# Kernel tuning notes

Hardware: AMD Instinct MI355X
Metric: run time of the kernel (lower is better)

## Reference

```python
import jax, jax.numpy as jnp
import numpy as np

THR = 10.0           # spike threshold (all layers, igarss2023 config)
LEAK1, LEAK2, LEAK3 = 9.0, 1.0, 0.0  # subtractive leak per layer
POOL1_K, POOL1_S = 7, 6
POOL2_K, POOL2_S = 2, 2
WTA_BLOCK = 2        # local spatial WTA window


def conv2d_same(x, w):
    # x: (B,C,H,W), w: (O,I,kh,kw)
    return jax.lax.conv_general_dilated(
        x, w, window_strides=(1, 1), padding='SAME',
        dimension_numbers=('NCHW', 'OIHW', 'NCHW'))


def maxpool(x, k, s):
    return jax.lax.reduce_window(
        x, -jnp.inf, jax.lax.max, (1, 1, k, k), (1, 1, s, s), 'VALID')


def wta(mem, spk, block=WTA_BLOCK):
    """Winner-take-all lateral inhibition ('both' mode):
    (1) channel competition: only the channel with max membrane at each
        spatial location may spike; (2) local spatial competition: only the
        max-membrane neuron within each block x block window of each map
        may spike. Requires H,W divisible by block."""
    C = mem.shape[1]
    ch_win = jnp.argmax(mem, axis=1)                         # (B,H,W)
    ch_mask = jax.nn.one_hot(ch_win, C, axis=1, dtype=mem.dtype)  # (B,C,H,W)
    loc = jax.lax.reduce_window(
        mem, -jnp.inf, jax.lax.max,
        (1, 1, block, block), (1, 1, block, block), 'VALID')
    loc_up = jnp.repeat(jnp.repeat(loc, block, axis=2), block, axis=3)
    sp_mask = (mem >= loc_up).astype(mem.dtype)
    return spk * ch_mask * sp_mask


def lif_step(mem, inp, leak, use_wta):
    # integrate -> threshold -> WTA -> reset-to-zero -> subtractive leak
    mem = mem + inp
    spk = (mem >= THR).astype(mem.dtype)
    if use_wta:
        spk = wta(mem, spk)
    mem = jnp.where(spk > 0, 0.0, mem)
    mem = jnp.maximum(mem - leak, 0.0)
    return mem, spk


def setup_inputs() -> dict:
    key = jax.random.key(0)
    k0, k1, k2, k3 = jax.random.split(key, 4)
    T, B, H, W = 20, 8, 256, 256
    x = jax.random.uniform(k0, (T, B, 1, H, W), dtype=jnp.float32)
    # STDP-style weights are non-negative in [0,1)
    w1 = jax.random.uniform(k1, (4, 1, 5, 5), dtype=jnp.float32)
    w2 = jax.random.uniform(k2, (36, 4, 5, 5), dtype=jnp.float32)
    w3 = jax.random.uniform(k3, (1, 36, 7, 7), dtype=jnp.float32)
    return {"x": x, "w1": w1, "w2": w2, "w3": w3}


def reference(x, w1, w2, w3):
    T, B, _, H, W = x.shape
    H1, W1 = H, W                                   # conv1 SAME
    H2 = (H1 - POOL1_K) // POOL1_S + 1              # 42
    W2 = (W1 - POOL1_K) // POOL1_S + 1
    H3 = (H2 - POOL2_K) // POOL2_S + 1              # 21
    W3 = (W2 - POOL2_K) // POOL2_S + 1
    C1, C2, C3 = w1.shape[0], w2.shape[0], w3.shape[0]

    m1_0 = jnp.zeros((B, C1, H1, W1), x.dtype)
    m2_0 = jnp.zeros((B, C2, H2, W2), x.dtype)
    m3_0 = jnp.zeros((B, C3, H3, W3), x.dtype)

    def step(carry, xt):
        m1, m2, m3 = carry
        m1, s1 = lif_step(m1, conv2d_same(xt, w1), LEAK1, True)
        p1 = maxpool(s1, POOL1_K, POOL1_S)
        m2, s2 = lif_step(m2, conv2d_same(p1, w2), LEAK2, True)
        p2 = maxpool(s2, POOL2_K, POOL2_S)
        m3, s3 = lif_step(m3, conv2d_same(p2, w3), LEAK3, False)
        return (m1, m2, m3), s3

    _, cls_spikes = jax.lax.scan(step, (m1_0, m2_0, m3_0), x)
    return cls_spikes  # (T, B, n_classes, H3, W3)
```

## Files before the change

### kernel.cpp

```cpp
#include <hip/hip_runtime.h>
#include <stdint.h>

#define THR 10.0f
#define AGT __HIP_MEMORY_SCOPE_AGENT

static constexpr size_t OFF_P2  = 2097152;
static constexpr size_t OFF_BAR = 2359296;

static __device__ __forceinline__ uint64_t ldu64(const uint64_t* p) {
    return __hip_atomic_load(p, __ATOMIC_RELAXED, AGT);
}
static __device__ __forceinline__ void stu64(uint64_t* p, uint64_t v) {
    __hip_atomic_store(p, v, __ATOMIC_RELAXED, AGT);
}

__global__ __launch_bounds__(256) void zero_bar(uint32_t* __restrict__ bar) {
    if (threadIdx.x < 256) bar[threadIdx.x] = 0u;
}

__device__ __forceinline__ void gbar(uint32_t* bar, int bid, uint32_t n) {
    __syncthreads();
    if (threadIdx.x == 0) {
        uint32_t* base = bar + (bid >> 6) * 32;
        uint32_t a = __hip_atomic_fetch_add(base, 1u, __ATOMIC_RELAXED, AGT);
        if (a == 64u * n - 1u)
            __hip_atomic_fetch_add(base + 16, 1u, __ATOMIC_RELAXED, AGT);
        while (__hip_atomic_load(base + 16, __ATOMIC_RELAXED, AGT) < n)
            __builtin_amdgcn_s_sleep(2);
    }
    __syncthreads();
}

__global__ __launch_bounds__(256, 2) void spike_persist(
    const float* __restrict__ x,
    const float* __restrict__ w1,
    const float* __restrict__ w2,
    const float* __restrict__ w3,
    float* __restrict__ out,
    uint8_t* __restrict__ s1b,
    uint8_t* __restrict__ p2b,
    uint32_t* __restrict__ bar)
{
    __shared__ union {
        float    xs[2112];
        uint64_t st64[279];
    } u;
    __shared__ uint64_t p2s[441];
    __shared__ float    ps[400];
    __shared__ float    mem_s[1296];
    __shared__ float    bm_s[324];
    __shared__ int      wc_s[36];
    __shared__ uint32_t p2a[18];

    const int tid = threadIdx.x;
    const int bid = blockIdx.x;
    uint32_t nbar = 0;

    const int b1 = bid >> 6;
    const int r0 = (bid & 63) * 4;
    const int tr = tid >> 7, tc = tid & 127;

    const int tIdx = bid & 63;
    const int b2 = bid >> 6;
    const int tyi = tIdx >> 3, txi = tIdx & 7;
    const int oy2 = tyi < 5 ? 6 * tyi : 30 + 4 * (tyi - 5);
    const int ox2 = txi < 5 ? 6 * txi : 30 + 4 * (txi - 5);
    const int th2 = tyi < 5 ? 6 : 4;
    const int tw2 = txi < 5 ? 6 : 4;
    const int wave = tid >> 6, lane = tid & 63;
    const int pr = lane / 6, pc = lane - 6 * pr;
    const bool act = (pr < th2) && (pc < tw2);
    const int prA = pr > 5 ? 0 : pr, pcA = pc;

    const int lid3 = (bid & 63) * 4 + wave;
    const int kyl = lane / 7, kxl = lane % 7;

    float w3v[36];
#pragma unroll
    for (int c = 0; c < 36; c++) w3v[c] = (lane < 49) ? w3[c * 49 + lane] : 0.f;

    int aoff[9]; uint32_t avalm = 0;
#pragma unroll
    for (int i = 0; i < 9; i++) {
        int idx = tid + i * 256;
        int row = idx / 264, col = idx - row * 264;
        int gy = r0 + row - 2, gx = col - 2;
        if ((idx < 2112) && gy >= 0 && gy < 256 && gx >= 0 && gx < 256)
            avalm |= 1u << i;
        aoff[i] = gy * 256 + gx;
    }
    const int s1soff64 = (b1 * 128 + (r0 >> 1) + tr) * 32 + (tc >> 2);

    const int rb0 = 3 * oy2 - 6;
    const int cb0 = (3 * ox2 - 6) >> 1;
    const int cq0 = cb0 >> 1;
    const int d16 = 2 * (cb0 & 1);
    int boff[2]; uint32_t bvalm = 0;
#pragma unroll
    for (int i = 0; i < 2; i++) {
        int idx = tid + i * 256;
        int row = idx / 9, q = idx - 9 * row;
        int grow = rb0 + row;
        int ucol = 2 * (cq0 + q);
        if ((idx < 279) && grow >= 0 && grow < 128 && ucol >= 0 && ucol < 64)
            bvalm |= 1u << i;
        boff[i] = (b2 * 128 + grow) * 32 + cq0 + q;
    }

    bool l3in[2], l3v[2]; int l3o[2];
#pragma unroll
    for (int rep = 0; rep < 2; rep++) {
        int o = lid3 + rep * 256;
        int rr = o / 21, cl = o - rr * 21;
        int yy = rr + kyl - 3, xx = cl + kxl - 3;
        l3in[rep] = o < 441;
        l3v[rep] = (o < 441) && (lane < 49) && yy >= 0 && yy < 21 && xx >= 0 && xx < 21;
        l3o[rep] = yy * 21 + xx;
    }

    float m1r[4][2][2];
#pragma unroll
    for (int c = 0; c < 4; c++)
#pragma unroll
        for (int dy = 0; dy < 2; dy++)
#pragma unroll
            for (int dx = 0; dx < 2; dx++) m1r[c][dy][dx] = 0.f;
    float m2r[9];
#pragma unroll
    for (int i = 0; i < 9; i++) m2r[i] = 0.f;
    float m3r[2] = {0.f, 0.f};

    for (int k = 0; k < 7; k++) {
        for (int tt = 0; tt < 4; tt++) {
            const int t = 4 * k + tt;
            if (t < 20) {
                uint64_t* s1w = reinterpret_cast<uint64_t*>(s1b + (size_t)(t & 7) * 262144);
                const float* xb = x + ((size_t)t * 8 + b1) * 65536;
                __syncthreads();
#pragma unroll
                for (int i = 0; i < 9; i++) {
                    int idx = tid + i * 256;
                    if (idx < 2112) u.xs[idx] = ((avalm >> i) & 1u) ? xb[aoff[i]] : 0.f;
                }
                __syncthreads();

                const float2* xs2 = reinterpret_cast<const float2*>(u.xs);
                float p[6][6];
#pragma unroll
                for (int i = 0; i < 6; i++)
#pragma unroll
                    for (int j = 0; j < 3; j++) {
                        float2 v = xs2[(2 * tr + i) * 132 + tc + j];
                        p[i][2 * j] = v.x; p[i][2 * j + 1] = v.y;
                    }

                float acc[4][2][2];
#pragma unroll
                for (int c = 0; c < 4; c++)
#pragma unroll
                    for (int dy = 0; dy < 2; dy++)
#pragma unroll
                        for (int dx = 0; dx < 2; dx++) acc[c][dy][dx] = 0.f;
#pragma unroll
                for (int c = 0; c < 4; c++)
#pragma unroll
                    for (int ky = 0; ky < 5; ky++)
#pragma unroll
                        for (int kx = 0; kx < 5; kx++) {
                            float w = w1[c * 25 + ky * 5 + kx];
#pragma unroll
                            for (int dy = 0; dy < 2; dy++)
#pragma unroll
                                for (int dx = 0; dx < 2; dx++)
                                    acc[c][dy][dx] = fmaf(p[dy + ky][dx + kx], w, acc[c][dy][dx]);
                        }

                float mem[4][2][2];
#pragma unroll
                for (int c = 0; c < 4; c++)
#pragma unroll
                    for (int dy = 0; dy < 2; dy++)
#pragma unroll
                        for (int dx = 0; dx < 2; dx++)
                            mem[c][dy][dx] = m1r[c][dy][dx] + acc[c][dy][dx];

                int wc[2][2];
#pragma unroll
                for (int dy = 0; dy < 2; dy++)
#pragma unroll
                    for (int dx = 0; dx < 2; dx++) {
                        int w = 0; float mx = mem[0][dy][dx];
#pragma unroll
                        for (int c = 1; c < 4; c++) {
                            float v = mem[c][dy][dx];
                            if (v > mx) { mx = v; w = c; }
                        }
                        wc[dy][dx] = w;
                    }

                float bm[4];
#pragma unroll
                for (int c = 0; c < 4; c++)
                    bm[c] = fmaxf(fmaxf(mem[c][0][0], mem[c][0][1]),
                                  fmaxf(mem[c][1][0], mem[c][1][1]));

                uint32_t bits = 0;
#pragma unroll
                for (int c = 0; c < 4; c++)
#pragma unroll
                    for (int dy = 0; dy < 2; dy++)
#pragma unroll
                        for (int dx = 0; dx < 2; dx++) {
                            float m = mem[c][dy][dx];
                            bool s = (m >= THR) && (wc[dy][dx] == c) && (m >= bm[c]);
                            m1r[c][dy][dx] = fmaxf((s ? 0.f : m) - 9.0f, 0.f);
                            bits |= (s ? 1u : 0u) << (c * 4 + dy * 2 + dx);
                        }
                uint32_t b32 = bits | ((uint32_t)__shfl_xor((int)bits, 1, 64) << 16);
                uint64_t b64 = (uint64_t)b32 |
                               ((uint64_t)(uint32_t)__shfl_xor((int)b32, 2, 64) << 32);
                if (!(tid & 3)) stu64(s1w + s1soff64, b64);
            }
        }

        uint64_t pf0 = 0, pf1 = 0;
        {
            int tb0 = 4 * k - 4;
            if (tb0 >= 0 && tb0 < 20) {
                const uint64_t* s1r64 = reinterpret_cast<const uint64_t*>(
                    s1b + (size_t)(tb0 & 7) * 262144);
                pf0 = (bvalm & 1u) ? ldu64(s1r64 + boff[0]) : 0ull;
                pf1 = (bvalm & 2u) ? ldu64(s1r64 + boff[1]) : 0ull;
            }
        }

        for (int tt = 0; tt < 4; tt++) {
            const int tl = 4 * k - 8 + tt;
            if (tl >= 0 && tl < 20) {
                const uint64_t* pb64 = reinterpret_cast<const uint64_t*>(
                    p2b + (size_t)(tl & 7) * 32768) + b2 * 441;
                __syncthreads();
                if (tid < 441) p2s[tid] = ldu64(pb64 + tid);
                {
                    int idx2 = tid + 256;
                    if (idx2 < 441) p2s[idx2] = ldu64(pb64 + idx2);
                }
                __syncthreads();
#pragma unroll
                for (int rep = 0; rep < 2; rep++) {
                    if (l3in[rep]) {
                        int o = lid3 + rep * 256;
                        uint64_t v = l3v[rep] ? p2s[l3o[rep]] : 0ull;
                        uint32_t lo = (uint32_t)v, hi = (uint32_t)(v >> 32);
                        float accv = 0.f;
#pragma unroll
                        for (int c = 0; c < 32; c++) accv += ((lo >> c) & 1u) ? w3v[c] : 0.f;
#pragma unroll
                        for (int c = 0; c < 4; c++)  accv += ((hi >> c) & 1u) ? w3v[32 + c] : 0.f;
#pragma unroll
                        for (int off = 32; off; off >>= 1) accv += __shfl_xor(accv, off, 64);
                        float memv3 = m3r[rep] + accv;
                        bool s = memv3 >= THR;
                        if (lane == 0) out[(size_t)tl * 3528 + b2 * 441 + o] = s ? 1.f : 0.f;
                        m3r[rep] = fmaxf(s ? 0.f : memv3, 0.f);
                    }
                }
            }
        }

        for (int tt = 0; tt < 4; tt++) {
            const int tb = 4 * k - 4 + tt;
            if (tb >= 0 && tb < 20) {
                uint64_t* p2w64 = reinterpret_cast<uint64_t*>(p2b + (size_t)(tb & 7) * 32768);

                __syncthreads();
                u.st64[tid] = pf0;
                {
                    int idx2 = tid + 256;
                    if (idx2 < 279) u.st64[idx2] = pf1;
                }
                {
                    int tbn = tb + 1;
                    if (tt < 3 && tbn < 20) {
                        const uint64_t* s1r64 = reinterpret_cast<const uint64_t*>(
                            s1b + (size_t)(tbn & 7) * 262144);
                        pf0 = (bvalm & 1u) ? ldu64(s1r64 + boff[0]) : 0ull;
                        pf1 = (bvalm & 2u) ? ldu64(s1r64 + boff[1]) : 0ull;
                    }
                }
                if (tid < 18) p2a[tid] = 0;
                __syncthreads();

                if (tid < 100) {
                    int r = tid / 10, cc2 = tid - 10 * (tid / 10);
                    int gy = oy2 - 2 + r, gx = ox2 - 2 + cc2;
                    uint32_t accb = 0;
                    if (r < th2 + 4 && cc2 < tw2 + 4 && gy >= 0 && gy < 42 && gx >= 0 && gx < 42) {
                        const uint16_t* st16 = reinterpret_cast<const uint16_t*>(u.st64);
#pragma unroll
                        for (int kr = 0; kr < 4; kr++)
#pragma unroll
                            for (int kc = 0; kc < 4; kc++) {
                                uint32_t m = (kr < 3) ? (kc < 3 ? 0xFu : 0x5u)
                                                      : (kc < 3 ? 0x3u : 0x1u);
                                uint32_t v = st16[(3 * r + kr) * 36 + 3 * cc2 + kc + d16];
                                accb |= v & (m * 0x1111u);
                            }
                    }
#pragma unroll
                    for (int ic = 0; ic < 4; ic++)
                        ps[ic * 100 + tid] = ((accb >> (4 * ic)) & 0xFu) ? 1.f : 0.f;
                }
                __syncthreads();

                float pv[4][5][5];
#pragma unroll
                for (int ic = 0; ic < 4; ic++)
#pragma unroll
                    for (int i = 0; i < 5; i++)
#pragma unroll
                        for (int j = 0; j < 5; j++)
                            pv[ic][i][j] = ps[ic * 100 + (prA + i) * 10 + (pcA + j)];

                float memv[9];
                for (int cc = 0; cc < 9; cc++) {
                    int c = cc * 4 + wave;
                    const float* wr = w2 + (size_t)__builtin_amdgcn_readfirstlane(c) * 100;
                    float accv = 0.f;
#pragma unroll
                    for (int ic = 0; ic < 4; ic++)
#pragma unroll
                        for (int i = 0; i < 5; i++)
#pragma unroll
                            for (int j = 0; j < 5; j++)
                                accv = fmaf(pv[ic][i][j], wr[ic * 25 + i * 5 + j], accv);
                    float m = act ? (m2r[cc] + accv) : -1e30f;
                    memv[cc] = m;
                    if (lane < 36) mem_s[c * 36 + lane] = m;
                }
                __syncthreads();

                if (tid < 36) {
                    float mx = mem_s[tid]; int w = 0;
#pragma unroll
                    for (int c = 1; c < 36; c++) {
                        float v = mem_s[c * 36 + tid];
                        if (v > mx) { mx = v; w = c; }
                    }
                    wc_s[tid] = w;
                }
#pragma unroll
                for (int i = 0; i < 2; i++) {
                    int idx = tid + i * 256;
                    if (idx < 324) {
                        int c = idx / 9, blk = idx - 9 * c;
                        int br = blk / 3, bc2 = blk - 3 * br;
                        int l0 = 12 * br + 2 * bc2;
                        float a = mem_s[c * 36 + l0],     bb2 = mem_s[c * 36 + l0 + 1];
                        float d = mem_s[c * 36 + l0 + 6], e   = mem_s[c * 36 + l0 + 7];
                        bm_s[idx] = fmaxf(fmaxf(a, bb2), fmaxf(d, e));
                    }
                }
                __syncthreads();

                const int blkl = (pr >> 1) * 3 + (pc >> 1);
                for (int cc = 0; cc < 9; cc++) {
                    int c = cc * 4 + wave;
                    if (act) {
                        float m = memv[cc];
                        bool s = (m >= THR) && (wc_s[lane] == c) && (m >= bm_s[c * 9 + blkl]);
                        m2r[cc] = fmaxf((s ? 0.f : m) - 1.0f, 0.f);
                    }
                }

#pragma unroll
                for (int i = 0; i < 2; i++) {
                    int idx = tid + i * 256;
                    if (idx < 324) {
                        int c = idx / 9, blk = idx - 9 * c;
                        int br = blk / 3, bc2 = blk - 3 * br;
                        if (2 * br < th2 && 2 * bc2 < tw2) {
                            int l0 = 12 * br + 2 * bc2;
                            float bmv = bm_s[idx];
                            bool any = false;
#pragma unroll
                            for (int kk = 0; kk < 4; kk++) {
                                int l = l0 + (kk >> 1) * 6 + (kk & 1);
                                float m = mem_s[c * 36 + l];
                                any |= (m >= THR) && (wc_s[l] == c) && (m >= bmv);
                            }
                            if (any)
                                atomicOr(&p2a[(blk << 1) + (c >> 5)], 1u << (c & 31));
                        }
                    }
                }
                __syncthreads();

                if (tid < 9) {
                    int br = tid / 3, bc2 = tid - 3 * br;
                    if (2 * br < th2 && 2 * bc2 < tw2) {
                        int cell = b2 * 441 + ((oy2 >> 1) + br) * 21 + (ox2 >> 1) + bc2;
                        uint64_t v = (uint64_t)p2a[tid * 2] |
                                     ((uint64_t)p2a[tid * 2 + 1] << 32);
                        stu64(p2w64 + cell, v);
                    }
                }
            }
        }

        if (k < 6) gbar(bar, bid, ++nbar);
    }
}

extern "C" void kernel_launch(void* const* d_in, const int* in_sizes, int n_in,
                              void* d_out, int out_size, void* d_ws, size_t ws_size,
                              hipStream_t stream) {
    const float* x  = (const float*)d_in[0];
    const float* w1 = (const float*)d_in[1];
    const float* w2 = (const float*)d_in[2];
    const float* w3 = (const float*)d_in[3];
    float* out = (float*)d_out;
    uint8_t* s1 = (uint8_t*)d_ws;
    uint8_t* p2 = (uint8_t*)d_ws + OFF_P2;
    uint32_t* bar = (uint32_t*)((char*)d_ws + OFF_BAR);

    zero_bar<<<1, 256, 0, stream>>>(bar);

    void* args[] = {(void*)&x, (void*)&w1, (void*)&w2, (void*)&w3,
                    (void*)&out, (void*)&s1, (void*)&p2, (void*)&bar};
    hipLaunchCooperativeKernel((void*)spike_persist, dim3(512), dim3(256),
                               args, 0, stream);
}
```

Before: 410.3 us.

## Warp-specialize persistent kernel so layer-1 and layer-2 stages run concurrently

Block size doubles to 512 threads. The first 256 threads handle layer-1 convolution and LIF plus layer-3 readout, and the second 256 handle layer-2 pooling, convolution and WTA. Each timestep interleaves both halves under shared __syncthreads, so stages that used to run one after another in the same block now overlap. Layer 3 now reads p2 straight from global memory instead of staging it in LDS, and the shared-memory union is split into separate buffers. This raises register and LDS pressure, and it adds barriers that both halves must hit even when only one half has work.

```diff
diff --git a/kernel.cpp b/kernel.cpp
--- a/kernel.cpp
+++ b/kernel.cpp
@@ -31,7 +31,7 @@
     __syncthreads();
 }
 
-__global__ __launch_bounds__(256, 2) void spike_persist(
+__global__ __launch_bounds__(512, 4) void spike_persist(
     const float* __restrict__ x,
     const float* __restrict__ w1,
     const float* __restrict__ w2,
@@ -41,11 +41,8 @@
     uint8_t* __restrict__ p2b,
     uint32_t* __restrict__ bar)
 {
-    __shared__ union {
-        float    xs[2112];
-        uint64_t st64[279];
-    } u;
-    __shared__ uint64_t p2s[441];
+    __shared__ float    xs[2112];
+    __shared__ uint64_t st64[279];
     __shared__ float    ps[400];
     __shared__ float    mem_s[1296];
     __shared__ float    bm_s[324];
@@ -54,97 +51,119 @@
 
     const int tid = threadIdx.x;
     const int bid = blockIdx.x;
+    const int bt = bid >> 6;
+    const bool isA = tid < 256;
+    const int btid = tid & 255;
+    const int wv = (tid >> 6) & 3;
+    const int lane = tid & 63;
     uint32_t nbar = 0;
 
-    const int b1 = bid >> 6;
-    const int r0 = (bid & 63) * 4;
-    const int tr = tid >> 7, tc = tid & 127;
-
-    const int tIdx = bid & 63;
-    const int b2 = bid >> 6;
-    const int tyi = tIdx >> 3, txi = tIdx & 7;
-    const int oy2 = tyi < 5 ? 6 * tyi : 30 + 4 * (tyi - 5);
-    const int ox2 = txi < 5 ? 6 * txi : 30 + 4 * (txi - 5);
-    const int th2 = tyi < 5 ? 6 : 4;
-    const int tw2 = txi < 5 ? 6 : 4;
-    const int wave = tid >> 6, lane = tid & 63;
-    const int pr = lane / 6, pc = lane - 6 * pr;
-    const bool act = (pr < th2) && (pc < tw2);
-    const int prA = pr > 5 ? 0 : pr, pcA = pc;
-
-    const int lid3 = (bid & 63) * 4 + wave;
-    const int kyl = lane / 7, kxl = lane % 7;
-
-    float w3v[36];
-#pragma unroll
-    for (int c = 0; c < 36; c++) w3v[c] = (lane < 49) ? w3[c * 49 + lane] : 0.f;
-
-    int aoff[9]; uint32_t avalm = 0;
-#pragma unroll
-    for (int i = 0; i < 9; i++) {
-        int idx = tid + i * 256;
-        int row = idx / 264, col = idx - row * 264;
-        int gy = r0 + row - 2, gx = col - 2;
-        if ((idx < 2112) && gy >= 0 && gy < 256 && gx >= 0 && gx < 256)
-            avalm |= 1u << i;
-        aoff[i] = gy * 256 + gx;
+    float m1r[4][2][2];
+    int aoff[9]; uint32_t avalm = 0; int s1soff64 = 0;
+    float w3v[36]; float m3r[2] = {0.f, 0.f};
+    bool l3in[2], l3v[2]; int l3o[2]; int lid3 = 0;
+    float m2r[9];
+    int boff[2]; uint32_t bvalm = 0; int d16 = 0;
+    int oy2 = 0, ox2 = 0, th2 = 0, tw2 = 0;
+    bool act = false; int prA = 0, pcA = 0;
+    uint64_t pf0 = 0, pf1 = 0;
+
+    if (isA) {
+        const int r0 = (bid & 63) * 4;
+        const int tr = tid >> 7, tc = tid & 127;
+#pragma unroll
+        for (int c = 0; c < 4; c++)
+#pragma unroll
+            for (int dy = 0; dy < 2; dy++)
+#pragma unroll
+                for (int dx = 0; dx < 2; dx++) m1r[c][dy][dx] = 0.f;
+#pragma unroll
+        for (int i = 0; i < 9; i++) {
+            int idx = tid + i * 256;
+            int row = idx / 264, col = idx - row * 264;
+            int gy = r0 + row - 2, gx = col - 2;
+            if ((idx < 2112) && gy >= 0 && gy < 256 && gx >= 0 && gx < 256)
+                avalm |= 1u << i;
+            aoff[i] = gy * 256 + gx;
+        }
+        s1soff64 = (bt * 128 + (r0 >> 1) + tr) * 32 + (tc >> 2);
+#pragma unroll
+        for (int c = 0; c < 36; c++) w3v[c] = (lane < 49) ? w3[c * 49 + lane] : 0.f;
+        lid3 = (bid & 63) * 4 + wv;
+        const int kyl = lane / 7, kxl = lane % 7;
+#pragma unroll
+        for (int rep = 0; rep < 2; rep++) {
+            int o = lid3 + rep * 256;
+            int rr = o / 21, cl = o - rr * 21;
+            int yy = rr + kyl - 3, xx = cl + kxl - 3;
+            l3in[rep] = o < 441;
+            l3v[rep] = (o < 441) && (lane < 49) && yy >= 0 && yy < 21 && xx >= 0 && xx < 21;
+            l3o[rep] = bt * 441 + yy * 21 + xx;
+        }
+    } else {
+        const int tIdx = bid & 63;
+        const int tyi = tIdx >> 3, txi = tIdx & 7;
+        oy2 = tyi < 5 ? 6 * tyi : 30 + 4 * (tyi - 5);
+        ox2 = txi < 5 ? 6 * txi : 30 + 4 * (txi - 5);
+        th2 = tyi < 5 ? 6 : 4;
+        tw2 = txi < 5 ? 6 : 4;
+        const int pr = lane / 6, pc = lane - 6 * pr;
+        act = (pr < th2) && (pc < tw2);
+        prA = pr > 5 ? 0 : pr; pcA = pc;
+#pragma unroll
+        for (int i = 0; i < 9; i++) m2r[i] = 0.f;
+        const int rb0 = 3 * oy2 - 6;
+        const int cb0 = (3 * ox2 - 6) >> 1;
+        const int cq0 = cb0 >> 1;
+        d16 = 2 * (cb0 & 1);
+#pragma unroll
+        for (int i = 0; i < 2; i++) {
+            int idx = btid + i * 256;
+            int row = idx / 9, q = idx - 9 * row;
+            int grow = rb0 + row;
+            int ucol = 2 * (cq0 + q);
+            if ((idx < 279) && grow >= 0 && grow < 128 && ucol >= 0 && ucol < 64)
+                bvalm |= 1u << i;
+            boff[i] = (bt * 128 + grow) * 32 + cq0 + q;
+        }
     }
-    const int s1soff64 = (b1 * 128 + (r0 >> 1) + tr) * 32 + (tc >> 2);
-
-    const int rb0 = 3 * oy2 - 6;
-    const int cb0 = (3 * ox2 - 6) >> 1;
-    const int cq0 = cb0 >> 1;
-    const int d16 = 2 * (cb0 & 1);
-    int boff[2]; uint32_t bvalm = 0;
-#pragma unroll
-    for (int i = 0; i < 2; i++) {
-        int idx = tid + i * 256;
-        int row = idx / 9, q = idx - 9 * row;
-        int grow = rb0 + row;
-        int ucol = 2 * (cq0 + q);
-        if ((idx < 279) && grow >= 0 && grow < 128 && ucol >= 0 && ucol < 64)
-            bvalm |= 1u << i;
-        boff[i] = (b2 * 128 + grow) * 32 + cq0 + q;
-    }
-
-    bool l3in[2], l3v[2]; int l3o[2];
-#pragma unroll
-    for (int rep = 0; rep < 2; rep++) {
-        int o = lid3 + rep * 256;
-        int rr = o / 21, cl = o - rr * 21;
-        int yy = rr + kyl - 3, xx = cl + kxl - 3;
-        l3in[rep] = o < 441;
-        l3v[rep] = (o < 441) && (lane < 49) && yy >= 0 && yy < 21 && xx >= 0 && xx < 21;
-        l3o[rep] = yy * 21 + xx;
-    }
-
-    float m1r[4][2][2];
-#pragma unroll
-    for (int c = 0; c < 4; c++)
-#pragma unroll
-        for (int dy = 0; dy < 2; dy++)
-#pragma unroll
-            for (int dx = 0; dx < 2; dx++) m1r[c][dy][dx] = 0.f;
-    float m2r[9];
-#pragma unroll
-    for (int i = 0; i < 9; i++) m2r[i] = 0.f;
-    float m3r[2] = {0.f, 0.f};
 
     for (int k = 0; k < 7; k++) {
+        if (!isA) {
+            int tb0 = 4 * k - 4;
+            if (tb0 >= 0 && tb0 < 20) {
+                const uint64_t* s1r64 = reinterpret_cast<const uint64_t*>(
+                    s1b + (size_t)(tb0 & 7) * 262144);
+                pf0 = (bvalm & 1u) ? ldu64(s1r64 + boff[0]) : 0ull;
+                pf1 = (bvalm & 2u) ? ldu64(s1r64 + boff[1]) : 0ull;
+            }
+        }
+
         for (int tt = 0; tt < 4; tt++) {
             const int t = 4 * k + tt;
-            if (t < 20) {
-                uint64_t* s1w = reinterpret_cast<uint64_t*>(s1b + (size_t)(t & 7) * 262144);
-                const float* xb = x + ((size_t)t * 8 + b1) * 65536;
-                __syncthreads();
+            const int tb = 4 * k - 4 + tt;
+            const int tl = 4 * k - 8 + tt;
+            const bool tok = t < 20;
+            const bool tbok = (tb >= 0) && (tb < 20);
+            const bool tlok = (tl >= 0) && (tl < 20);
+
+            if (isA && tok) {
+                const float* xb = x + ((size_t)t * 8 + bt) * 65536;
 #pragma unroll
                 for (int i = 0; i < 9; i++) {
                     int idx = tid + i * 256;
-                    if (idx < 2112) u.xs[idx] = ((avalm >> i) & 1u) ? xb[aoff[i]] : 0.f;
-                }
-                __syncthreads();
-
-                const float2* xs2 = reinterpret_cast<const float2*>(u.xs);
+                    if (idx < 2112) xs[idx] = ((avalm >> i) & 1u) ? xb[aoff[i]] : 0.f;
+                }
+            } else if (!isA && tbok) {
+                st64[btid] = pf0;
+                if (btid + 256 < 279) st64[btid + 256] = pf1;
+            }
+            __syncthreads();
+
+            if (isA && tok) {
+                uint64_t* s1w = reinterpret_cast<uint64_t*>(s1b + (size_t)(t & 7) * 262144);
+                const int tr = tid >> 7, tc = tid & 127;
+                const float2* xs2 = reinterpret_cast<const float2*>(xs);
                 float p[6][6];
 #pragma unroll
                 for (int i = 0; i < 6; i++)
@@ -220,83 +239,13 @@
                 uint64_t b64 = (uint64_t)b32 |
                                ((uint64_t)(uint32_t)__shfl_xor((int)b32, 2, 64) << 32);
                 if (!(tid & 3)) stu64(s1w + s1soff64, b64);
-            }
-        }
-
-        uint64_t pf0 = 0, pf1 = 0;
-        {
-            int tb0 = 4 * k - 4;
-            if (tb0 >= 0 && tb0 < 20) {
-                const uint64_t* s1r64 = reinterpret_cast<const uint64_t*>(
-                    s1b + (size_t)(tb0 & 7) * 262144);
-                pf0 = (bvalm & 1u) ? ldu64(s1r64 + boff[0]) : 0ull;
-                pf1 = (bvalm & 2u) ? ldu64(s1r64 + boff[1]) : 0ull;
-            }
-        }
-
-        for (int tt = 0; tt < 4; tt++) {
-            const int tl = 4 * k - 8 + tt;
-            if (tl >= 0 && tl < 20) {
-                const uint64_t* pb64 = reinterpret_cast<const uint64_t*>(
-                    p2b + (size_t)(tl & 7) * 32768) + b2 * 441;
-                __syncthreads();
-                if (tid < 441) p2s[tid] = ldu64(pb64 + tid);
-                {
-                    int idx2 = tid + 256;
-                    if (idx2 < 441) p2s[idx2] = ldu64(pb64 + idx2);
-                }
-                __syncthreads();
-#pragma unroll
-                for (int rep = 0; rep < 2; rep++) {
-                    if (l3in[rep]) {
-                        int o = lid3 + rep * 256;
-                        uint64_t v = l3v[rep] ? p2s[l3o[rep]] : 0ull;
-                        uint32_t lo = (uint32_t)v, hi = (uint32_t)(v >> 32);
-                        float accv = 0.f;
-#pragma unroll
-                        for (int c = 0; c < 32; c++) accv += ((lo >> c) & 1u) ? w3v[c] : 0.f;
-#pragma unroll
-                        for (int c = 0; c < 4; c++)  accv += ((hi >> c) & 1u) ? w3v[32 + c] : 0.f;
-#pragma unroll
-                        for (int off = 32; off; off >>= 1) accv += __shfl_xor(accv, off, 64);
-                        float memv3 = m3r[rep] + accv;
-                        bool s = memv3 >= THR;
-                        if (lane == 0) out[(size_t)tl * 3528 + b2 * 441 + o] = s ? 1.f : 0.f;
-                        m3r[rep] = fmaxf(s ? 0.f : memv3, 0.f);
-                    }
-                }
-            }
-        }
-
-        for (int tt = 0; tt < 4; tt++) {
-            const int tb = 4 * k - 4 + tt;
-            if (tb >= 0 && tb < 20) {
-                uint64_t* p2w64 = reinterpret_cast<uint64_t*>(p2b + (size_t)(tb & 7) * 32768);
-
-                __syncthreads();
-                u.st64[tid] = pf0;
-                {
-                    int idx2 = tid + 256;
-                    if (idx2 < 279) u.st64[idx2] = pf1;
-                }
-                {
-                    int tbn = tb + 1;
-                    if (tt < 3 && tbn < 20) {
-                        const uint64_t* s1r64 = reinterpret_cast<const uint64_t*>(
-                            s1b + (size_t)(tbn & 7) * 262144);
-                        pf0 = (bvalm & 1u) ? ldu64(s1r64 + boff[0]) : 0ull;
-                        pf1 = (bvalm & 2u) ? ldu64(s1r64 + boff[1]) : 0ull;
-                    }
-                }
-                if (tid < 18) p2a[tid] = 0;
-                __syncthreads();
-
-                if (tid < 100) {
-                    int r = tid / 10, cc2 = tid - 10 * (tid / 10);
+            } else if (!isA && tbok) {
+                if (btid < 100) {
+                    int r = btid / 10, cc2 = btid - 10 * (btid / 10);
                     int gy = oy2 - 2 + r, gx = ox2 - 2 + cc2;
                     uint32_t accb = 0;
                     if (r < th2 + 4 && cc2 < tw2 + 4 && gy >= 0 && gy < 42 && gx >= 0 && gx < 42) {
-                        const uint16_t* st16 = reinterpret_cast<const uint16_t*>(u.st64);
+                        const uint16_t* st16 = reinterpret_cast<const uint16_t*>(st64);
 #pragma unroll
                         for (int kr = 0; kr < 4; kr++)
 #pragma unroll
@@ -309,10 +258,34 @@
                     }
 #pragma unroll
                     for (int ic = 0; ic < 4; ic++)
-                        ps[ic * 100 + tid] = ((accb >> (4 * ic)) & 0xFu) ? 1.f : 0.f;
-                }
-                __syncthreads();
-
+                        ps[ic * 100 + btid] = ((accb >> (4 * ic)) & 0xFu) ? 1.f : 0.f;
+                }
+            }
+            __syncthreads();
+
+            if (isA && tlok) {
+                const uint64_t* pb64 = reinterpret_cast<const uint64_t*>(
+                    p2b + (size_t)(tl & 7) * 32768);
+#pragma unroll
+                for (int rep = 0; rep < 2; rep++) {
+                    if (l3in[rep]) {
+                        int o = lid3 + rep * 256;
+                        uint64_t v = l3v[rep] ? ldu64(pb64 + l3o[rep]) : 0ull;
+                        uint32_t lo = (uint32_t)v, hi = (uint32_t)(v >> 32);
+                        float accv = 0.f;
+#pragma unroll
+                        for (int c = 0; c < 32; c++) accv += ((lo >> c) & 1u) ? w3v[c] : 0.f;
+#pragma unroll
+                        for (int c = 0; c < 4; c++)  accv += ((hi >> c) & 1u) ? w3v[32 + c] : 0.f;
+#pragma unroll
+                        for (int off = 32; off; off >>= 1) accv += __shfl_xor(accv, off, 64);
+                        float memv3 = m3r[rep] + accv;
+                        bool s = memv3 >= THR;
+                        if (lane == 0) out[(size_t)tl * 3528 + bt * 441 + o] = s ? 1.f : 0.f;
+                        m3r[rep] = fmaxf(s ? 0.f : memv3, 0.f);
+                    }
+                }
+            } else if (!isA && tbok) {
                 float pv[4][5][5];
 #pragma unroll
                 for (int ic = 0; ic < 4; ic++)
@@ -322,9 +295,18 @@
                         for (int j = 0; j < 5; j++)
                             pv[ic][i][j] = ps[ic * 100 + (prA + i) * 10 + (pcA + j)];
 
-                float memv[9];
+                {
+                    int tbn = tb + 1;
+                    if (tt < 3 && tbn >= 0 && tbn < 20) {
+                        const uint64_t* s1r64 = reinterpret_cast<const uint64_t*>(
+                            s1b + (size_t)(tbn & 7) * 262144);
+                        pf0 = (bvalm & 1u) ? ldu64(s1r64 + boff[0]) : 0ull;
+                        pf1 = (bvalm & 2u) ? ldu64(s1r64 + boff[1]) : 0ull;
+                    }
+                }
+
                 for (int cc = 0; cc < 9; cc++) {
-                    int c = cc * 4 + wave;
+                    int c = cc * 4 + wv;
                     const float* wr = w2 + (size_t)__builtin_amdgcn_readfirstlane(c) * 100;
                     float accv = 0.f;
 #pragma unroll
@@ -335,23 +317,24 @@
                             for (int j = 0; j < 5; j++)
                                 accv = fmaf(pv[ic][i][j], wr[ic * 25 + i * 5 + j], accv);
                     float m = act ? (m2r[cc] + accv) : -1e30f;
-                    memv[cc] = m;
                     if (lane < 36) mem_s[c * 36 + lane] = m;
                 }
-                __syncthreads();
-
-                if (tid < 36) {
-                    float mx = mem_s[tid]; int w = 0;
+            }
+            __syncthreads();
+
+            if (!isA && tbok) {
+                if (btid < 36) {
+                    float mx = mem_s[btid]; int w = 0;
 #pragma unroll
                     for (int c = 1; c < 36; c++) {
-                        float v = mem_s[c * 36 + tid];
+                        float v = mem_s[c * 36 + btid];
                         if (v > mx) { mx = v; w = c; }
                     }
-                    wc_s[tid] = w;
+                    wc_s[btid] = w;
                 }
 #pragma unroll
                 for (int i = 0; i < 2; i++) {
-                    int idx = tid + i * 256;
+                    int idx = btid + i * 256;
                     if (idx < 324) {
                         int c = idx / 9, blk = idx - 9 * c;
                         int br = blk / 3, bc2 = blk - 3 * br;
@@ -361,21 +344,24 @@
                         bm_s[idx] = fmaxf(fmaxf(a, bb2), fmaxf(d, e));
                     }
                 }
-                __syncthreads();
-
+                if (btid < 18) p2a[btid] = 0;
+            }
+            __syncthreads();
+
+            if (!isA && tbok) {
+                const int pr = lane / 6, pc = lane - 6 * pr;
                 const int blkl = (pr >> 1) * 3 + (pc >> 1);
                 for (int cc = 0; cc < 9; cc++) {
-                    int c = cc * 4 + wave;
+                    int c = cc * 4 + wv;
                     if (act) {
-                        float m = memv[cc];
+                        float m = mem_s[c * 36 + lane];
                         bool s = (m >= THR) && (wc_s[lane] == c) && (m >= bm_s[c * 9 + blkl]);
                         m2r[cc] = fmaxf((s ? 0.f : m) - 1.0f, 0.f);
                     }
                 }
-
 #pragma unroll
                 for (int i = 0; i < 2; i++) {
-                    int idx = tid + i * 256;
+                    int idx = btid + i * 256;
                     if (idx < 324) {
                         int c = idx / 9, blk = idx - 9 * c;
                         int br = blk / 3, bc2 = blk - 3 * br;
@@ -394,14 +380,18 @@
                         }
                     }
                 }
-                __syncthreads();
-
-                if (tid < 9) {
-                    int br = tid / 3, bc2 = tid - 3 * br;
+            }
+            __syncthreads();
+
+            if (!isA && tbok) {
+                if (btid < 9) {
+                    int br = btid / 3, bc2 = btid - 3 * br;
                     if (2 * br < th2 && 2 * bc2 < tw2) {
-                        int cell = b2 * 441 + ((oy2 >> 1) + br) * 21 + (ox2 >> 1) + bc2;
-                        uint64_t v = (uint64_t)p2a[tid * 2] |
-                                     ((uint64_t)p2a[tid * 2 + 1] << 32);
+                        uint64_t* p2w64 = reinterpret_cast<uint64_t*>(
+                            p2b + (size_t)(tb & 7) * 32768);
+                        int cell = bt * 441 + ((oy2 >> 1) + br) * 21 + (ox2 >> 1) + bc2;
+                        uint64_t v = (uint64_t)p2a[btid * 2] |
+                                     ((uint64_t)p2a[btid * 2 + 1] << 32);
                         stu64(p2w64 + cell, v);
                     }
                 }
@@ -428,6 +418,6 @@
 
     void* args[] = {(void*)&x, (void*)&w1, (void*)&w2, (void*)&w3,
                     (void*)&out, (void*)&s1, (void*)&p2, (void*)&bar};
-    hipLaunchCooperativeKernel((void*)spike_persist, dim3(512), dim3(256),
+    hipLaunchCooperativeKernel((void*)spike_persist, dim3(512), dim3(512),
                                args, 0, stream);
 }
```

Measured after the change: 849.7 us. +107.1%, slower.
